# Optimization experiments

Hardware: AMD Instinct MI355X
Metric: run time of the kernel (lower is better)

The kernel has to match this reference:

```python
import jax, jax.numpy as jnp
import numpy as np


def setup_inputs() -> dict:
    key = jax.random.key(0)
    k1, k2, k3, k4, k5 = jax.random.split(key, 5)
    B, K, S, E, I, D = 4, 2, 512, 8, 1024, 2048
    x = jax.random.normal(k1, (B, S, I), dtype=jnp.float32)
    weights = jax.random.uniform(k2, (B, K, S), dtype=jnp.float32)
    ensembles = jax.random.randint(k3, (B, K, S), 0, E, dtype=jnp.int64)
    # xavier_uniform-style init for expert weight tables
    lim1 = float(np.sqrt(6.0 / (D + I)))
    proj_in = jax.random.uniform(k4, (E, D, I), dtype=jnp.float32, minval=-lim1, maxval=lim1)
    proj_out = jax.random.uniform(k5, (E, I, D), dtype=jnp.float32, minval=-lim1, maxval=lim1)
    return {"x": x, "weights": weights, "ensembles": ensembles,
            "proj_in": proj_in, "proj_out": proj_out}


def reference(x, weights, ensembles, proj_in, proj_out):
    # x: (B,S,I); weights/ensembles: (B,K,S); proj_in: (E,D,I); proj_out: (E,I,D)
    # Same math as the torch module (dropout = identity in eval):
    #   per token t, out = sum_k w[k,t] * W2[e_kt] @ relu(W1[e_kt] @ x[t])
    # Computed as all-expert batched GEMMs + a gated (one-hot scatter) combine,
    # which is mathematically identical and avoids the (B,K,S,D,I) gather blowup.
    E = proj_in.shape[0]
    h = jax.nn.relu(jnp.einsum('edi,bsi->bsed', proj_in, x))      # (B,S,E,D)
    o = jnp.einsum('eid,bsed->bsei', proj_out, h)                 # (B,S,E,I)
    onehot = jax.nn.one_hot(ensembles, E, dtype=x.dtype)          # (B,K,S,E)
    gate = jnp.einsum('bks,bkse->bse', weights, onehot)           # (B,S,E)
    return jnp.einsum('bsei,bse->bsi', o, gate)                   # (B,S,I)
```

## Files before the change

kernel.cpp:

```cpp
#include <hip/hip_runtime.h>
#include <stdint.h>

#define THREADS 512
#define GRID1 (8 * 3 * 8)
#define NE 8
#define BB 4
#define SS 512
#define KK 2
#define II 1024
#define DD 2048
#define NTOK (BB * SS)
#define NASSIGN (BB * KK * SS)

#define F4_X (NTOK * II / 4)
#define F4_P (NE * DD * II / 4)
#define CVB_X (F4_X / 1024)
#define CVB_P (F4_P / 1024)
#define CVA_TOTAL (CVB_X + CVB_P)
#define CVH_P (F4_P / 2048)

typedef unsigned short u16;
typedef __attribute__((ext_vector_type(8))) __bf16 bf16x8;
typedef __attribute__((ext_vector_type(4))) float f32x4;
typedef __attribute__((ext_vector_type(4))) unsigned int u32x4;

__device__ __forceinline__ u16 f32_to_bf16(float f) {
    unsigned int u = __builtin_bit_cast(unsigned int, f);
    unsigned int r = u + 0x7FFFu + ((u >> 16) & 1u);
    return (u16)(r >> 16);
}

__device__ __forceinline__ unsigned int pk2(float a, float b) {
    return (unsigned int)f32_to_bf16(a) | ((unsigned int)f32_to_bf16(b) << 16);
}

__device__ __forceinline__ void gload16(const void* g, void* l) {
    __builtin_amdgcn_global_load_lds(
        (const __attribute__((address_space(1))) unsigned int*)g,
        (__attribute__((address_space(3))) unsigned int*)l, 16, 0, 0);
}

#define BARRIER() do { \
    __builtin_amdgcn_sched_barrier(0); \
    __builtin_amdgcn_s_barrier(); \
    __builtin_amdgcn_sched_barrier(0); } while (0)

__device__ void setup_body(const void* __restrict__ ens_raw,
                           const float* __restrict__ weights,
                           int* __restrict__ meta,
                           int* __restrict__ tok,
                           float* __restrict__ wgt) {
    __shared__ int s_cnt[NE];
    __shared__ int s_cur[NE];
    __shared__ int s_flag;
    const int t = threadIdx.x;
    if (t < NE) s_cnt[t] = 0;
    if (t == 0) s_flag = 0;
    __syncthreads();

    const unsigned int* w32 = (const unsigned int*)ens_raw;
    unsigned int f = 0;
    for (int i = t; i < NASSIGN / 2; i += 256) f |= w32[2 * i + 1];
    if (f) atomicOr(&s_flag, 1);
    __syncthreads();
    const bool is32 = (s_flag != 0);
    const int* e32 = (const int*)ens_raw;
    const long long* e64 = (const long long*)ens_raw;

    for (int a = t; a < NASSIGN; a += 256) {
        int e = is32 ? e32[a] : (int)e64[a];
        atomicAdd(&s_cnt[e & 7], 1);
    }
    __syncthreads();

    if (t == 0) {
        int pb = 0, nt = 0;
        for (int e = 0; e < NE; e++) {
            int c = s_cnt[e];
            meta[8 + e] = c;
            meta[16 + e] = pb;
            s_cur[e] = pb;
            int n128 = (c + 127) >> 7;
            int pe = pb + n128 * 128;
            for (int i2 = 0; i2 < n128; i2 += 2) {
                meta[32 + nt] = e;
                meta[64 + nt] = pb + i2 * 128;
                meta[96 + nt] = pb + c;
                meta[128 + nt] = pe;
                nt++;
            }
            pb = pe;
        }
        meta[0] = nt;
        meta[1] = pb;
    }
    __syncthreads();

    for (int a = t; a < NASSIGN; a += 256) {
        int e = is32 ? e32[a] : (int)e64[a];
        e &= 7;
        int slot = atomicAdd(&s_cur[e], 1);
        int b = a >> 10;
        int s = a & (SS - 1);
        tok[slot] = b * SS + s;
        wgt[slot] = weights[a];
    }
    __syncthreads();

    for (int e = 0; e < NE; e++) {
        int st = meta[16 + e] + meta[8 + e];
        int en = (e < NE - 1) ? meta[16 + e + 1] : meta[1];
        for (int i = st + t; i < en; i += 256) {
            tok[i] = 0;
            wgt[i] = 0.f;
        }
    }
}

__global__ __launch_bounds__(256)
void convert_setup(const float* __restrict__ x,
                   const float* __restrict__ pin,
                   u16* __restrict__ xb,
                   u16* __restrict__ pb1,
                   const void* __restrict__ ens,
                   const float* __restrict__ weights,
                   int* __restrict__ meta,
                   int* __restrict__ tok,
                   float* __restrict__ wgt) {
    const int b = blockIdx.x;
    if (b >= CVA_TOTAL) {
        setup_body(ens, weights, meta, tok, wgt);
        return;
    }
    const float* s;
    u16* d;
    size_t base;
    if (b < CVB_X) { s = x;   d = xb;  base = (size_t)b * 1024; }
    else           { s = pin; d = pb1; base = (size_t)(b - CVB_X) * 1024; }
    const f32x4* s4 = (const f32x4*)s;
    f32x4 v[4];
#pragma unroll
    for (int q = 0; q < 4; q++)
        v[q] = __builtin_nontemporal_load(&s4[base + q * 256 + threadIdx.x]);
#pragma unroll
    for (int q = 0; q < 4; q++) {
        uint2 o;
        o.x = pk2(v[q][0], v[q][1]);
        o.y = pk2(v[q][2], v[q][3]);
        *(uint2*)(d + 4 * (base + q * 256 + threadIdx.x)) = o;
    }
}

__global__ __launch_bounds__(THREADS, 2)
void gemm1(const u16* __restrict__ Abase,
           const u16* __restrict__ Bbase,
           const int* __restrict__ meta,
           const int* __restrict__ tok,
           u16* __restrict__ hdst,
           const float* __restrict__ pout,
           u16* __restrict__ pout_bf) {
    constexpr int NT = II / 64;
    constexpr int ASZ = 256 * 64 * 2;
    constexpr int BUFSZ = 2 * ASZ;
    __shared__ char smem[2 * BUFSZ];

    const int lid = blockIdx.x;
    if (lid >= GRID1) {
        const size_t base = (size_t)(lid - GRID1) * 2048;
        const f32x4* s4 = (const f32x4*)pout;
        f32x4 v[4];
#pragma unroll
        for (int q = 0; q < 4; q++)
            v[q] = __builtin_nontemporal_load(&s4[base + q * 512 + threadIdx.x]);
#pragma unroll
        for (int q = 0; q < 4; q++) {
            uint2 o;
            o.x = pk2(v[q][0], v[q][1]);
            o.y = pk2(v[q][2], v[q][3]);
            *(uint2*)(pout_bf + 4 * (base + q * 512 + threadIdx.x)) = o;
        }
        return;
    }

    const int g = lid & 7;
    const int i = lid >> 3;
    const int tile = g + 8 * (i % 3);
    const int colt = i / 3;
    if (tile >= meta[0]) return;

    const int e     = meta[32 + tile];
    const int sbase = meta[64 + tile];
    const int wend  = meta[128 + tile];
    const int padmax = meta[1];
    const int colbase = colt * 256;

    const int tid = threadIdx.x;
    const int lane = tid & 63;
    const int wv = tid >> 6;
    const int wr = wv >> 2;
    const int wc = wv & 3;

    const u16* Bp = Bbase + (size_t)e * (size_t)(DD * II) + (size_t)colbase * II;

    int aoff[4], boff[4], cdst[4];
#pragma unroll
    for (int j = 0; j < 4; j++) {
        int c = j * 512 + tid;
        int row = c >> 3;
        int s = (c & 7) ^ (row & 7);
        cdst[j] = c * 16;
        int slot = sbase + row;
        if (slot > padmax - 1) slot = padmax - 1;
        aoff[j] = tok[slot] * II + s * 8;
        boff[j] = row * II + s * 8;
    }

    f32x4 acc[8][4];
#pragma unroll
    for (int m = 0; m < 8; m++)
#pragma unroll
        for (int n = 0; n < 4; n++)
            acc[m][n] = (f32x4){0.f, 0.f, 0.f, 0.f};

    auto STAGE = [&](int kt, char* buf) {
        const int kof = kt * 64;
#pragma unroll
        for (int j = 0; j < 4; j++)
            gload16(Abase + aoff[j] + kof, buf + cdst[j]);
#pragma unroll
        for (int j = 0; j < 4; j++)
            gload16(Bp + boff[j] + kof, buf + ASZ + cdst[j]);
    };

    auto COMPUTE = [&](const char* buf) {
        const u16* As = (const u16*)buf;
        const u16* Bs = (const u16*)(buf + ASZ);
#pragma unroll
        for (int kk = 0; kk < 2; kk++) {
            bf16x8 a[8], b[4];
#pragma unroll
            for (int m = 0; m < 8; m++) {
                int row = wr * 128 + m * 16 + (lane & 15);
                int slot = (kk * 4 + (lane >> 4)) ^ (row & 7);
                a[m] = *(const bf16x8*)&As[row * 64 + slot * 8];
            }
#pragma unroll
            for (int n = 0; n < 4; n++) {
                int col = wc * 64 + n * 16 + (lane & 15);
                int slot = (kk * 4 + (lane >> 4)) ^ (col & 7);
                b[n] = *(const bf16x8*)&Bs[col * 64 + slot * 8];
            }
            asm volatile("s_waitcnt lgkmcnt(0)" ::: "memory");
            __builtin_amdgcn_sched_barrier(0);
            __builtin_amdgcn_s_setprio(1);
#pragma unroll
            for (int m = 0; m < 8; m++)
#pragma unroll
                for (int n = 0; n < 4; n++)
                    acc[m][n] = __builtin_amdgcn_mfma_f32_16x16x32_bf16(
                        a[m], b[n], acc[m][n], 0, 0, 0);
            __builtin_amdgcn_s_setprio(0);
        }
    };

    char* buf0 = smem;
    char* buf1 = smem + BUFSZ;

    STAGE(0, buf0);
    asm volatile("s_waitcnt vmcnt(0)" ::: "memory");
    BARRIER();

#pragma unroll 1
    for (int t = 0; t < NT; ++t) {
        char* cur = (t & 1) ? buf1 : buf0;
        char* nxt = (t & 1) ? buf0 : buf1;
        const bool st = (t + 1 < NT);
        if (st) STAGE(t + 1, nxt);
        COMPUTE(cur);
        if (st) asm volatile("s_waitcnt vmcnt(0)" ::: "memory");
        BARRIER();
    }

#pragma unroll
    for (int m = 0; m < 8; m++) {
#pragma unroll
        for (int r = 0; r < 4; r++) {
            int row = wr * 128 + m * 16 + (lane >> 4) * 4 + r;
            int slot = sbase + row;
            if (slot < wend) {
                size_t ro = (size_t)slot * DD;
#pragma unroll
                for (int n = 0; n < 4; n++) {
                    int col = colbase + wc * 64 + n * 16 + (lane & 15);
                    float v = acc[m][n][r];
                    v = v > 0.f ? v : 0.f;
                    hdst[ro + col] = f32_to_bf16(v);
                }
            }
        }
    }
}

__global__ __launch_bounds__(THREADS, 2)
void gemm2(const u16* __restrict__ Abase,
           const u16* __restrict__ Bbase,
           const int* __restrict__ meta,
           const int* __restrict__ tok,
           const float* __restrict__ wgt,
           float* __restrict__ outdst) {
    constexpr int NT = DD / 64;
    constexpr int ASZ = 256 * 64 * 2;
    constexpr int BSZ = 128 * 64 * 2;
    constexpr int BUFSZ = ASZ + BSZ;
    __shared__ char smem[3 * BUFSZ];

    const int lid = blockIdx.x;
    const int g = lid & 7;
    const int i = lid >> 3;
    const int tile = g + 8 * (i % 3);
    const int colt = i / 3;
    if (tile >= meta[0]) return;

    const int e     = meta[32 + tile];
    const int sbase = meta[64 + tile];
    const int rend  = meta[96 + tile];
    const int padmax = meta[1];
    const int colbase = colt * 128;

    const int tid = threadIdx.x;
    const int lane = tid & 63;
    const int wv = tid >> 6;
    const int wr = wv >> 1;
    const int wc = wv & 1;

    const u16* Bp = Bbase + (size_t)e * (size_t)(DD * II) + (size_t)colbase * DD;

    int aoff[4], adst[4], boff[2], bdst[2];
#pragma unroll
    for (int j = 0; j < 4; j++) {
        int c = j * 512 + tid;
        int row = c >> 3;
        int s = (c & 7) ^ (row & 7);
        adst[j] = c * 16;
        int slot = sbase + row;
        if (slot > padmax - 1) slot = padmax - 1;
        aoff[j] = slot * DD + s * 8;
    }
#pragma unroll
    for (int j = 0; j < 2; j++) {
        int c = j * 512 + tid;
        int row = c >> 3;
        int s = (c & 7) ^ (row & 7);
        bdst[j] = c * 16;
        boff[j] = row * DD + s * 8;
    }

    f32x4 acc[4][4];
#pragma unroll
    for (int m = 0; m < 4; m++)
#pragma unroll
        for (int n = 0; n < 4; n++)
            acc[m][n] = (f32x4){0.f, 0.f, 0.f, 0.f};

    auto STAGE = [&](int kt, char* buf) {
        const int kof = kt * 64;
#pragma unroll
        for (int j = 0; j < 4; j++)
            gload16(Abase + aoff[j] + kof, buf + adst[j]);
#pragma unroll
        for (int j = 0; j < 2; j++)
            gload16(Bp + boff[j] + kof, buf + ASZ + bdst[j]);
    };

    auto COMPUTE = [&](const char* buf) {
        const u16* As = (const u16*)buf;
        const u16* Bs = (const u16*)(buf + ASZ);
        bf16x8 a[2][4], b[2][4];
#pragma unroll
        for (int kk = 0; kk < 2; kk++) {
#pragma unroll
            for (int m = 0; m < 4; m++) {
                int row = wr * 64 + m * 16 + (lane & 15);
                int slot = (kk * 4 + (lane >> 4)) ^ (row & 7);
                a[kk][m] = *(const bf16x8*)&As[row * 64 + slot * 8];
            }
#pragma unroll
            for (int n = 0; n < 4; n++) {
                int col = wc * 64 + n * 16 + (lane & 15);
                int slot = (kk * 4 + (lane >> 4)) ^ (col & 7);
                b[kk][n] = *(const bf16x8*)&Bs[col * 64 + slot * 8];
            }
        }
        asm volatile("s_waitcnt lgkmcnt(0)" ::: "memory");
        __builtin_amdgcn_sched_barrier(0);
        __builtin_amdgcn_s_setprio(1);
#pragma unroll
        for (int m = 0; m < 4; m++)
#pragma unroll
            for (int n = 0; n < 4; n++) {
                acc[m][n] = __builtin_amdgcn_mfma_f32_16x16x32_bf16(
                    a[0][m], b[0][n], acc[m][n], 0, 0, 0);
                acc[m][n] = __builtin_amdgcn_mfma_f32_16x16x32_bf16(
                    a[1][m], b[1][n], acc[m][n], 0, 0, 0);
            }
        __builtin_amdgcn_s_setprio(0);
    };

    char* pA = smem;
    char* pB = smem + BUFSZ;
    char* pC = smem + 2 * BUFSZ;

    STAGE(0, pA);
    STAGE(1, pB);
    asm volatile("s_waitcnt vmcnt(6)" ::: "memory");
    BARRIER();

#pragma unroll 1
    for (int t = 0; t < NT; ++t) {
        const bool st = (t + 2 < NT);
        if (st) STAGE(t + 2, pC);
        COMPUTE(pA);
        if (st) {
            asm volatile("s_waitcnt vmcnt(6)" ::: "memory");
        } else if (t + 1 < NT) {
            asm volatile("s_waitcnt vmcnt(0)" ::: "memory");
        }
        BARRIER();
        { char* tp = pA; pA = pB; pB = pC; pC = tp; }
    }

#pragma unroll
    for (int m = 0; m < 4; m++) {
#pragma unroll
        for (int r = 0; r < 4; r++) {
            int row = wr * 64 + m * 16 + (lane >> 4) * 4 + r;
            int slot = sbase + row;
            if (slot < rend) {
                float w = wgt[slot];
                size_t obase = (size_t)tok[slot] * II;
#pragma unroll
                for (int n = 0; n < 4; n++) {
                    int col = colbase + wc * 64 + n * 16 + (lane & 15);
                    atomicAdd(&outdst[obase + col], acc[m][n][r] * w);
                }
            }
        }
    }
}

extern "C" void kernel_launch(void* const* d_in, const int* in_sizes, int n_in,
                              void* d_out, int out_size, void* d_ws, size_t ws_size,
                              hipStream_t stream) {
    const float* x = (const float*)d_in[0];
    const float* weights = (const float*)d_in[1];
    const void* ens = d_in[2];
    const float* pin = (const float*)d_in[3];
    const float* pout = (const float*)d_in[4];
    float* out = (float*)d_out;

    char* ws = (char*)d_ws;
    int*   meta    = (int*)(ws);
    int*   tok     = (int*)(ws + 1024);
    float* wgt     = (float*)(ws + 21504);
    u16*   x_bf    = (u16*)(ws + 41984);
    u16*   pin_bf  = (u16*)(ws + 4236288);
    u16*   pout_bf = (u16*)(ws + 37790720);
    u16*   h       = (u16*)(ws + 71345152);

    hipMemsetAsync(d_out, 0, (size_t)out_size * sizeof(float), stream);

    convert_setup<<<dim3(CVA_TOTAL + 1), dim3(256), 0, stream>>>(
        x, pin, x_bf, pin_bf, ens, weights, meta, tok, wgt);

    gemm1<<<dim3(GRID1 + CVH_P), dim3(THREADS), 0, stream>>>(
        x_bf, pin_bf, meta, tok, h, pout, pout_bf);

    gemm2<<<dim3(8 * 3 * 8), dim3(THREADS), 0, stream>>>(
        h, pout_bf, meta, tok, wgt, out);
}
```

Measured before the change: 120.8 us.

## Replace gemm2 atomic scatter with per-slot stores and a gather-reduce kernel

gemm2 now writes each routed slot's output row to a float scratch buffer with plain non-temporal stores instead of atomically adding weighted results into the output. A new reduce_out kernel uses an inverse token-to-slot map, built during setup, to combine each token's two expert outputs with their gate weights. This removes the output memset and the float atomics. In exchange it adds an extra kernel launch and a full write plus read of the slot buffer, which reuses the pin_bf workspace region.

```diff
diff --git a/kernel.cpp b/kernel.cpp
--- a/kernel.cpp
+++ b/kernel.cpp
@@ -49,7 +49,8 @@
                            const float* __restrict__ weights,
                            int* __restrict__ meta,
                            int* __restrict__ tok,
-                           float* __restrict__ wgt) {
+                           float* __restrict__ wgt,
+                           int* __restrict__ inv) {
     __shared__ int s_cnt[NE];
     __shared__ int s_cur[NE];
     __shared__ int s_flag;
@@ -101,9 +102,12 @@
         e &= 7;
         int slot = atomicAdd(&s_cur[e], 1);
         int b = a >> 10;
+        int k = (a >> 9) & 1;
         int s = a & (SS - 1);
-        tok[slot] = b * SS + s;
+        int token = b * SS + s;
+        tok[slot] = token;
         wgt[slot] = weights[a];
+        inv[token * 2 + k] = slot;
     }
     __syncthreads();
 
@@ -126,10 +130,11 @@
                    const float* __restrict__ weights,
                    int* __restrict__ meta,
                    int* __restrict__ tok,
-                   float* __restrict__ wgt) {
+                   float* __restrict__ wgt,
+                   int* __restrict__ inv) {
     const int b = blockIdx.x;
     if (b >= CVA_TOTAL) {
-        setup_body(ens, weights, meta, tok, wgt);
+        setup_body(ens, weights, meta, tok, wgt, inv);
         return;
     }
     const float* s;
@@ -305,9 +310,7 @@
 void gemm2(const u16* __restrict__ Abase,
            const u16* __restrict__ Bbase,
            const int* __restrict__ meta,
-           const int* __restrict__ tok,
-           const float* __restrict__ wgt,
-           float* __restrict__ outdst) {
+           float* __restrict__ o_slot) {
     constexpr int NT = DD / 64;
     constexpr int ASZ = 256 * 64 * 2;
     constexpr int BSZ = 128 * 64 * 2;
@@ -436,16 +439,37 @@
             int row = wr * 64 + m * 16 + (lane >> 4) * 4 + r;
             int slot = sbase + row;
             if (slot < rend) {
-                float w = wgt[slot];
-                size_t obase = (size_t)tok[slot] * II;
+                float* orow = o_slot + (size_t)slot * II + colbase;
 #pragma unroll
                 for (int n = 0; n < 4; n++) {
-                    int col = colbase + wc * 64 + n * 16 + (lane & 15);
-                    atomicAdd(&outdst[obase + col], acc[m][n][r] * w);
+                    int col = wc * 64 + n * 16 + (lane & 15);
+                    __builtin_nontemporal_store(acc[m][n][r], orow + col);
                 }
             }
         }
     }
+}
+
+__global__ __launch_bounds__(256)
+void reduce_out(const float* __restrict__ o_slot,
+                const int* __restrict__ inv,
+                const float* __restrict__ wgt,
+                float* __restrict__ out) {
+    const int t = blockIdx.x;
+    const int s0 = inv[2 * t];
+    const int s1 = inv[2 * t + 1];
+    const float w0 = wgt[s0];
+    const float w1 = wgt[s1];
+    const f32x4* r0 = (const f32x4*)(o_slot + (size_t)s0 * II);
+    const f32x4* r1 = (const f32x4*)(o_slot + (size_t)s1 * II);
+    f32x4* o = (f32x4*)(out + (size_t)t * II);
+    const int c = threadIdx.x;
+    f32x4 a = r0[c];
+    f32x4 b = r1[c];
+    f32x4 v;
+#pragma unroll
+    for (int j = 0; j < 4; j++) v[j] = w0 * a[j] + w1 * b[j];
+    __builtin_nontemporal_store(v, &o[c]);
 }
 
 extern "C" void kernel_launch(void* const* d_in, const int* in_sizes, int n_in,
@@ -462,19 +486,21 @@
     int*   meta    = (int*)(ws);
     int*   tok     = (int*)(ws + 1024);
     float* wgt     = (float*)(ws + 21504);
-    u16*   x_bf    = (u16*)(ws + 41984);
-    u16*   pin_bf  = (u16*)(ws + 4236288);
-    u16*   pout_bf = (u16*)(ws + 37790720);
-    u16*   h       = (u16*)(ws + 71345152);
-
-    hipMemsetAsync(d_out, 0, (size_t)out_size * sizeof(float), stream);
+    int*   inv     = (int*)(ws + 41984);
+    u16*   x_bf    = (u16*)(ws + 58368);
+    u16*   pin_bf  = (u16*)(ws + 4252672);
+    u16*   pout_bf = (u16*)(ws + 37807104);
+    u16*   h       = (u16*)(ws + 71361536);
+    float* o_slot  = (float*)(ws + 4252672);
 
     convert_setup<<<dim3(CVA_TOTAL + 1), dim3(256), 0, stream>>>(
-        x, pin, x_bf, pin_bf, ens, weights, meta, tok, wgt);
+        x, pin, x_bf, pin_bf, ens, weights, meta, tok, wgt, inv);
 
     gemm1<<<dim3(GRID1 + CVH_P), dim3(THREADS), 0, stream>>>(
         x_bf, pin_bf, meta, tok, h, pout, pout_bf);
 
     gemm2<<<dim3(8 * 3 * 8), dim3(THREADS), 0, stream>>>(
-        h, pout_bf, meta, tok, wgt, out);
-}
+        h, pout_bf, meta, o_slot);
+
+    reduce_out<<<dim3(NTOK), dim3(256), 0, stream>>>(o_slot, inv, wgt, out);
+}
```

New measurement: 112.0 us (median of 2 runs). -7.3%, faster.
